# Performance work log

Measured on AMD Instinct MI355X. Metric: run time of the kernel, lower is better.

## Reference

```python
import jax, jax.numpy as jnp
import numpy as np

N_QUBITS = 10
QLCU_LAYERS = 2
GATE_LAYERS = 2
FEATURE_DIM = 256
OUTPUT_DIM = 1
BATCH = 2048
TWO_PI = float(2.0 * np.pi)
N_MEAS = 3 * N_QUBITS


def _ang(theta, B):
    # broadcast scalar or (B,) angle to (B,) float32
    return jnp.broadcast_to(jnp.asarray(theta, jnp.float32), (B,))


def _apply_1q(psi, U, wire):
    # psi: (B,)+(2,)*n ; U: (B,2,2) complex64
    pm = jnp.moveaxis(psi, wire + 1, -1)
    out = jnp.einsum('bij,b...j->b...i', U, pm)
    return jnp.moveaxis(out, -1, wire + 1)


def rx(psi, theta, wire):
    B = psi.shape[0]
    t = _ang(theta, B) * 0.5
    c = jnp.cos(t).astype(jnp.complex64)
    s = (-1j) * jnp.sin(t).astype(jnp.complex64)
    U = jnp.stack([jnp.stack([c, s], -1), jnp.stack([s, c], -1)], -2)
    return _apply_1q(psi, U, wire)


def ry(psi, theta, wire):
    B = psi.shape[0]
    t = _ang(theta, B) * 0.5
    c = jnp.cos(t).astype(jnp.complex64)
    s = jnp.sin(t).astype(jnp.complex64)
    U = jnp.stack([jnp.stack([c, -s], -1), jnp.stack([s, c], -1)], -2)
    return _apply_1q(psi, U, wire)


def rz(psi, theta, wire):
    # diagonal: e^{-i t/2}, e^{+i t/2}
    B = psi.shape[0]
    n = psi.ndim - 1
    t = _ang(theta, B) * 0.5
    ph = jnp.exp(1j * jnp.stack([-t, t], -1).astype(jnp.complex64))  # (B,2)
    pm = jnp.moveaxis(psi, wire + 1, -1)
    pm = pm * ph.reshape((B,) + (1,) * (n - 1) + (2,))
    return jnp.moveaxis(pm, -1, wire + 1)


def _mv2(psi, a, b):
    return jnp.moveaxis(psi, (a + 1, b + 1), (-2, -1))


def _mv2_back(pm, a, b):
    return jnp.moveaxis(pm, (-2, -1), (a + 1, b + 1))


def crz(psi, theta, control, target):
    # diagonal on (control,target): [1, 1, e^{-it/2}, e^{+it/2}]
    B = psi.shape[0]
    n = psi.ndim - 1
    t = (_ang(theta, B) * 0.5).astype(jnp.complex64)
    e_m = jnp.exp(-1j * t)
    e_p = jnp.exp(1j * t)
    one = jnp.ones_like(e_m)
    P = jnp.stack([jnp.stack([one, one], -1), jnp.stack([e_m, e_p], -1)], -2)  # (B,2,2)
    pm = _mv2(psi, control, target)
    pm = pm * P.reshape((B,) + (1,) * (n - 2) + (2, 2))
    return _mv2_back(pm, control, target)


def ising_xx(psi, theta, a, b):
    # exp(-i t/2 XX): cos(t/2) I - i sin(t/2) X(x)X (bit-flip both)
    B = psi.shape[0]
    n = psi.ndim - 1
    t = _ang(theta, B) * 0.5
    c = jnp.cos(t).astype(jnp.complex64).reshape((B,) + (1,) * n)
    s = jnp.sin(t).astype(jnp.complex64).reshape((B,) + (1,) * n)
    pm = _mv2(psi, a, b)
    out = c * pm - 1j * s * pm[..., ::-1, ::-1]
    return _mv2_back(out, a, b)


def ising_yy(psi, theta, a, b):
    # exp(-i t/2 YY): (YY psi)[ta,tb] = (-1 if ta==tb else +1) * psi[flip]
    B = psi.shape[0]
    n = psi.ndim - 1
    t = _ang(theta, B) * 0.5
    c = jnp.cos(t).astype(jnp.complex64).reshape((B,) + (1,) * n)
    s = jnp.sin(t).astype(jnp.complex64).reshape((B,) + (1,) * n)
    sign = jnp.array([[-1.0, 1.0], [1.0, -1.0]], jnp.complex64)
    pm = _mv2(psi, a, b)
    out = c * pm - 1j * s * sign * pm[..., ::-1, ::-1]
    return _mv2_back(out, a, b)


def measure_xyz(psi):
    # expvals [X0..X_{n-1}, Y0.., Z0..] -> (B, 3n) float32
    n = psi.ndim - 1
    xs, ys, zs = [], [], []
    for w in range(n):
        pm = jnp.moveaxis(psi, w + 1, -1)
        p0, p1 = pm[..., 0], pm[..., 1]
        axes = tuple(range(1, n))
        a = jnp.sum(jnp.conj(p0) * p1, axis=axes)
        xs.append(2.0 * jnp.real(a))
        ys.append(2.0 * jnp.imag(a))
        zs.append(jnp.sum(jnp.abs(p0) ** 2 - jnp.abs(p1) ** 2, axis=axes))
    return jnp.stack(xs + ys + zs, axis=1).astype(jnp.float32)


def selective_ssm(psi, qlcu, bpar, cpar, dtpar, n, layers):
    idx = 0
    for _ in range(layers):
        for i in range(n):
            psi = ry(psi, qlcu[:, idx], i); idx += 1
        for i in range(n):
            psi = ising_xx(psi, qlcu[:, idx], i, (i + 1) % n); idx += 1
        for i in range(n):
            psi = ry(psi, bpar[i], i)
        for i in range(n):
            psi = ry(psi, qlcu[:, idx], i); idx += 1
        for i in range(n):
            psi = ising_yy(psi, qlcu[:, idx], i, (i + 1) % n); idx += 1
        for i in range(n):
            psi = rz(psi, cpar[i], i)
        for i in range(n):
            psi = rx(psi, dtpar[i], i)
    return psi


def gating(psi, gp, n, layers):
    idx = 0
    for _ in range(layers):
        for i in range(n):
            psi = rx(psi, gp[idx], i); idx += 1
        for i in range(n - 1):
            psi = crz(psi, gp[idx], i, i + 1); idx += 1
        for i in range(n):
            psi = ry(psi, gp[idx], i); idx += 1
        if n > 1:
            psi = crz(psi, gp[idx], n - 1, 0); idx += 1
    return psi


def skip_circuit(psi, sp, n):
    idx = 0
    for i in range(n):
        psi = rx(psi, sp[idx], i); idx += 1
    for i in range(n):
        psi = ry(psi, sp[idx], i); idx += 1
    for i in range(n):
        psi = rz(psi, sp[idx], i); idx += 1
    return psi


def _forward(x, W_proj, b_proj, qlcu_base, gate_base, skip_base, b_params, c_params, dt_params,
             W1, b1, W2, b2, W3, b3, w1, w2, w3, W_out, b_out):
    B = x.shape[0]
    n = N_QUBITS
    proj = x @ W_proj.T + b_proj
    qlcu = jax.nn.sigmoid(proj) * TWO_PI + qlcu_base[None, :]
    psi0 = jnp.zeros((B, 2 ** n), jnp.complex64).at[:, 0].set(1.0).reshape((B,) + (2,) * n)
    m1 = measure_xyz(selective_ssm(psi0, qlcu, b_params, c_params, dt_params, n, QLCU_LAYERS))
    # branches 2/3 have batch-independent params and initial state -> compute once, broadcast
    psi1 = jnp.zeros((1, 2 ** n), jnp.complex64).at[:, 0].set(1.0).reshape((1,) + (2,) * n)
    m2 = jnp.broadcast_to(measure_xyz(gating(psi1, gate_base, n, GATE_LAYERS)), (B, N_MEAS))
    m3 = jnp.broadcast_to(measure_xyz(skip_circuit(psi1, skip_base, n)), (B, N_MEAS))
    y1 = m1 @ W1.T + b1
    y2 = m2 @ W2.T + b2
    y3 = m3 @ W3.T + b3
    comb = w1 * y1 + w2 * y2 + w3 * y3
    return comb @ W_out.T + b_out


def setup_inputs() -> dict:
    key = jax.random.key(0)
    ks = jax.random.split(key, 17)
    nq = N_QUBITS
    n_qlcu = 4 * nq * QLCU_LAYERS
    n_gate = 4 * nq * GATE_LAYERS
    n_skip = 3 * nq
    lim_p = 1.0 / np.sqrt(FEATURE_DIM)
    lim_m = 1.0 / np.sqrt(N_MEAS)
    return dict(
        x=jax.random.normal(ks[0], (BATCH, FEATURE_DIM), jnp.float32),
        W_proj=jax.random.uniform(ks[1], (n_qlcu, FEATURE_DIM), jnp.float32, -lim_p, lim_p),
        b_proj=jax.random.uniform(ks[2], (n_qlcu,), jnp.float32, -lim_p, lim_p),
        qlcu_base=jax.random.uniform(ks[3], (n_qlcu,), jnp.float32, 0.0, TWO_PI),
        gate_base=jax.random.uniform(ks[4], (n_gate,), jnp.float32, 0.0, TWO_PI),
        skip_base=jax.random.uniform(ks[5], (n_skip,), jnp.float32, 0.0, TWO_PI),
        b_params=jax.random.uniform(ks[6], (nq,), jnp.float32, 0.0, TWO_PI),
        c_params=jax.random.uniform(ks[7], (nq,), jnp.float32, 0.0, TWO_PI),
        dt_params=jax.random.uniform(ks[8], (nq,), jnp.float32, 0.0, TWO_PI),
        W1=jax.random.uniform(ks[9], (N_MEAS, N_MEAS), jnp.float32, -lim_m, lim_m),
        b1=jax.random.uniform(ks[10], (N_MEAS,), jnp.float32, -lim_m, lim_m),
        W2=jax.random.uniform(ks[11], (N_MEAS, N_MEAS), jnp.float32, -lim_m, lim_m),
        b2=jax.random.uniform(ks[12], (N_MEAS,), jnp.float32, -lim_m, lim_m),
        W3=jax.random.uniform(ks[13], (N_MEAS, N_MEAS), jnp.float32, -lim_m, lim_m),
        b3=jax.random.uniform(ks[14], (N_MEAS,), jnp.float32, -lim_m, lim_m),
        w1=jnp.ones((1,), jnp.float32),
        w2=jnp.ones((1,), jnp.float32),
        w3=jnp.ones((1,), jnp.float32),
        W_out=jax.random.uniform(ks[15], (OUTPUT_DIM, N_MEAS), jnp.float32, -lim_m, lim_m),
        b_out=jax.random.uniform(ks[16], (OUTPUT_DIM,), jnp.float32, -lim_m, lim_m),
    )


def reference(x, W_proj, b_proj, qlcu_base, gate_base, skip_base, b_params, c_params, dt_params,
              W1, b1, W2, b2, W3, b3, w1, w2, w3, W_out, b_out):
    return _forward(x, W_proj, b_proj, qlcu_base, gate_base, skip_base, b_params, c_params, dt_params,
                    W1, b1, W2, b2, W3, b3, w1, w2, w3, W_out, b_out)
```

## Files before the change

kernel.cpp:

```cpp
#include <hip/hip_runtime.h>
#include <math.h>

#define TPB 320
#define TWO_PI_F 6.283185307179586f


#define ALLQ(OP) OP(0) OP(1) OP(2) OP(3) OP(4) OP(5) OP(6) OP(7) OP(8) OP(9)
#define ALLQ9(OP) OP(0) OP(1) OP(2) OP(3) OP(4) OP(5) OP(6) OP(7) OP(8)

template<int CTRL>
__device__ __forceinline__ float dppmv(float v) {
    return __builtin_bit_cast(float,
        __builtin_amdgcn_update_dpp(0, __builtin_bit_cast(int, v), CTRL, 0xF, 0xF, true));
}

template<int LM>
__device__ __forceinline__ float lx(float v, int lane) {
    (void)lane;
    if constexpr (LM == 1)       return dppmv<0xB1>(v);
    else if constexpr (LM == 2)  return dppmv<0x4E>(v);
    else if constexpr (LM == 3)  return dppmv<0x1B>(v);
    else if constexpr (LM == 4)  return dppmv<0x1B>(dppmv<0x141>(v));
    else if constexpr (LM == 6)  return dppmv<0xB1>(dppmv<0x141>(v));
    else if constexpr (LM == 8)  return dppmv<0x128>(v);
    else if constexpr (LM == 12) return dppmv<0x1B>(dppmv<0x140>(v));
    else                         return __shfl_xor(v, LM);
}


template<int W>
__device__ __forceinline__ void g_ry(float (&re)[16], float (&im)[16], float c, float s, int lane) {
    if constexpr (W <= 5) {
        constexpr int LM = 1 << (5 - W);
        const float ss = ((lane >> (5 - W)) & 1) ? s : -s;
        float pr[16], pi[16];
#pragma unroll
        for (int r = 0; r < 16; ++r) { pr[r] = lx<LM>(re[r], lane); pi[r] = lx<LM>(im[r], lane); }
#pragma unroll
        for (int r = 0; r < 16; ++r) {
            re[r] = fmaf(ss, pr[r], c * re[r]);
            im[r] = fmaf(ss, pi[r], c * im[r]);
        }
    } else {
        constexpr int MK = 1 << (9 - W);
#pragma unroll
        for (int r = 0; r < 16; ++r) {
            if ((r & MK) == 0) {
                const int r1 = r | MK;
                float r0 = re[r], i0 = im[r], r1v = re[r1], i1 = im[r1];
                re[r]  = fmaf(-s, r1v, c * r0);
                im[r]  = fmaf(-s, i1,  c * i0);
                re[r1] = fmaf( s, r0,  c * r1v);
                im[r1] = fmaf( s, i0,  c * i1);
            }
        }
    }
}

template<int W>
__device__ __forceinline__ void g_rx(float (&re)[16], float (&im)[16], float c, float s, int lane) {
    if constexpr (W <= 5) {
        constexpr int LM = 1 << (5 - W);
        float pr[16], pi[16];
#pragma unroll
        for (int r = 0; r < 16; ++r) { pr[r] = lx<LM>(re[r], lane); pi[r] = lx<LM>(im[r], lane); }
#pragma unroll
        for (int r = 0; r < 16; ++r) {
            re[r] = fmaf( s, pi[r], c * re[r]);
            im[r] = fmaf(-s, pr[r], c * im[r]);
        }
    } else {
        constexpr int MK = 1 << (9 - W);
#pragma unroll
        for (int r = 0; r < 16; ++r) {
            if ((r & MK) == 0) {
                const int r1 = r | MK;
                float r0 = re[r], i0 = im[r], r1v = re[r1], i1 = im[r1];
                re[r]  = fmaf( s, i1,  c * r0);
                im[r]  = fmaf(-s, r1v, c * i0);
                re[r1] = fmaf( s, i0,  c * r1v);
                im[r1] = fmaf(-s, r0,  c * i1);
            }
        }
    }
}

template<int W>
__device__ __forceinline__ void g_rz(float (&re)[16], float (&im)[16], float c, float s, int lane) {
    if constexpr (W <= 5) {
        const float sp = ((lane >> (5 - W)) & 1) ? s : -s;
#pragma unroll
        for (int r = 0; r < 16; ++r) {
            float rr = re[r], ii = im[r];
            re[r] = rr * c - ii * sp;
            im[r] = ii * c + rr * sp;
        }
    } else {
        constexpr int MK = 1 << (9 - W);
#pragma unroll
        for (int r = 0; r < 16; ++r) {
            const float sp = (r & MK) ? s : -s;
            float rr = re[r], ii = im[r];
            re[r] = rr * c - ii * sp;
            im[r] = ii * c + rr * sp;
        }
    }
}

template<int C, int T>
__device__ __forceinline__ void g_crz(float (&re)[16], float (&im)[16], float c, float s, int lane) {
#pragma unroll
    for (int r = 0; r < 16; ++r) {
        const int cb = (C <= 5) ? ((lane >> (5 - C)) & 1) : ((r >> (9 - C)) & 1);
        const int tb = (T <= 5) ? ((lane >> (5 - T)) & 1) : ((r >> (9 - T)) & 1);
        const float cc  = cb ? c : 1.f;
        const float sp2 = cb ? (tb ? s : -s) : 0.f;
        float rr = re[r], ii = im[r];
        re[r] = cc * rr - sp2 * ii;
        im[r] = cc * ii + sp2 * rr;
    }
}

template<int A, int Bq, bool YY>
__device__ __forceinline__ void g_xy(float (&re)[16], float (&im)[16], float c, float s, int lane) {
    constexpr int bpA = 9 - A, bpB = 9 - Bq;
    constexpr int LM   = ((bpA >= 4) ? (1 << (bpA - 4)) : 0) | ((bpB >= 4) ? (1 << (bpB - 4)) : 0);
    constexpr int LOCM = ((bpA < 4) ? (1 << bpA) : 0) | ((bpB < 4) ? (1 << bpB) : 0);
    float pr[16], pi[16];
#pragma unroll
    for (int r = 0; r < 16; ++r) {
        float vr = re[r ^ LOCM], vi = im[r ^ LOCM];
        if constexpr (LM != 0) { pr[r] = lx<LM>(vr, lane); pi[r] = lx<LM>(vi, lane); }
        else                   { pr[r] = vr; pi[r] = vi; }
    }
#pragma unroll
    for (int r = 0; r < 16; ++r) {
        float sg;
        if constexpr (YY) {
            const int bA = (A  <= 5) ? ((lane >> (5 - A )) & 1) : ((r >> (9 - A )) & 1);
            const int bB = (Bq <= 5) ? ((lane >> (5 - Bq)) & 1) : ((r >> (9 - Bq)) & 1);
            sg = (bA == bB) ? -s : s;
        } else sg = s;
        float rr = re[r], ii = im[r];
        re[r] = fmaf( sg, pi[r], c * rr);
        im[r] = fmaf(-sg, pr[r], c * ii);
    }
}

template<int W>
__device__ __forceinline__ void g_u1(float (&re)[16], float (&im)[16], const float* U, int lane) {
    const float u00r=U[0], u00i=U[1], u01r=U[2], u01i=U[3];
    const float u10r=U[4], u10i=U[5], u11r=U[6], u11i=U[7];
    if constexpr (W <= 5) {
        constexpr int LM = 1 << (5 - W);
        const int side = (lane >> (5 - W)) & 1;
        const float aR = side ? u11r : u00r, aI = side ? u11i : u00i;
        const float bR = side ? u10r : u01r, bI = side ? u10i : u01i;
        float pr[16], pi[16];
#pragma unroll
        for (int r = 0; r < 16; ++r) { pr[r] = lx<LM>(re[r], lane); pi[r] = lx<LM>(im[r], lane); }
#pragma unroll
        for (int r = 0; r < 16; ++r) {
            float rr = re[r], ii = im[r];
            float nr = aR * rr; nr = fmaf(-aI, ii, nr); nr = fmaf(bR, pr[r], nr); nr = fmaf(-bI, pi[r], nr);
            float ni = aR * ii; ni = fmaf( aI, rr, ni); ni = fmaf(bR, pi[r], ni); ni = fmaf( bI, pr[r], ni);
            re[r] = nr; im[r] = ni;
        }
    } else {
        constexpr int MK = 1 << (9 - W);
#pragma unroll
        for (int r = 0; r < 16; ++r) {
            if ((r & MK) == 0) {
                const int r1 = r | MK;
                float r0 = re[r], i0 = im[r], r1v = re[r1], i1 = im[r1];
                float a = u00r*r0; a = fmaf(-u00i, i0, a); a = fmaf(u01r, r1v, a); a = fmaf(-u01i, i1, a);
                float b = u00r*i0; b = fmaf( u00i, r0, b); b = fmaf(u01r, i1,  b); b = fmaf( u01i, r1v, b);
                float c = u10r*r0; c = fmaf(-u10i, i0, c); c = fmaf(u11r, r1v, c); c = fmaf(-u11i, i1, c);
                float d = u10r*i0; d = fmaf( u10i, r0, d); d = fmaf(u11r, i1,  d); d = fmaf( u11i, r1v, d);
                re[r] = a; im[r] = b; re[r1] = c; im[r1] = d;
            }
        }
    }
}


__device__ __forceinline__ void g_ry2_01(float (&re)[16], float (&im)[16],
                                         float c0, float s0, float c1, float s1, int lane) {
    float ar[16], ai[16], br[16], bi[16], cr2[16], ci2[16];
#pragma unroll
    for (int r = 0; r < 16; ++r) { ar[r] = lx<32>(re[r], lane); ai[r] = lx<32>(im[r], lane); }
#pragma unroll
    for (int r = 0; r < 16; ++r) { br[r] = lx<16>(re[r], lane); bi[r] = lx<16>(im[r], lane); }
#pragma unroll
    for (int r = 0; r < 16; ++r) { cr2[r] = lx<48>(re[r], lane); ci2[r] = lx<48>(im[r], lane); }
    const float sg0 = ((lane >> 5) & 1) ? s0 : -s0;
    const float sg1 = ((lane >> 4) & 1) ? s1 : -s1;
    const float k0 = c0 * c1, k1 = c1 * sg0, k2 = c0 * sg1, k3 = sg0 * sg1;
#pragma unroll
    for (int r = 0; r < 16; ++r) {
        float o_r = k0 * re[r];
        o_r = fmaf(k1, ar[r], o_r); o_r = fmaf(k2, br[r], o_r); o_r = fmaf(k3, cr2[r], o_r);
        float o_i = k0 * im[r];
        o_i = fmaf(k1, ai[r], o_i); o_i = fmaf(k2, bi[r], o_i); o_i = fmaf(k3, ci2[r], o_i);
        re[r] = o_r; im[r] = o_i;
    }
}

__device__ __forceinline__ void g_u2_01(float (&re)[16], float (&im)[16],
                                        const float* U0, const float* U1, int lane) {
    const int b0 = (lane >> 5) & 1, b1 = (lane >> 4) & 1;
    const float u0o_r = U0[(b0*2+b0)*2],       u0o_i = U0[(b0*2+b0)*2+1];
    const float u0f_r = U0[(b0*2+(b0^1))*2],   u0f_i = U0[(b0*2+(b0^1))*2+1];
    const float u1o_r = U1[(b1*2+b1)*2],       u1o_i = U1[(b1*2+b1)*2+1];
    const float u1f_r = U1[(b1*2+(b1^1))*2],   u1f_i = U1[(b1*2+(b1^1))*2+1];
    const float K00r = u0o_r*u1o_r - u0o_i*u1o_i, K00i = u0o_r*u1o_i + u0o_i*u1o_r;
    const float K01r = u0o_r*u1f_r - u0o_i*u1f_i, K01i = u0o_r*u1f_i + u0o_i*u1f_r;
    const float K10r = u0f_r*u1o_r - u0f_i*u1o_i, K10i = u0f_r*u1o_i + u0f_i*u1o_r;
    const float K11r = u0f_r*u1f_r - u0f_i*u1f_i, K11i = u0f_r*u1f_i + u0f_i*u1f_r;
    float ar[16], ai[16], br[16], bi[16], cr2[16], ci2[16];
#pragma unroll
    for (int r = 0; r < 16; ++r) { ar[r] = lx<32>(re[r], lane); ai[r] = lx<32>(im[r], lane); }
#pragma unroll
    for (int r = 0; r < 16; ++r) { br[r] = lx<16>(re[r], lane); bi[r] = lx<16>(im[r], lane); }
#pragma unroll
    for (int r = 0; r < 16; ++r) { cr2[r] = lx<48>(re[r], lane); ci2[r] = lx<48>(im[r], lane); }
#pragma unroll
    for (int r = 0; r < 16; ++r) {
        float rr = re[r], ii = im[r];
        float o_r = K00r * rr;         o_r = fmaf(-K00i, ii, o_r);
        o_r = fmaf(K01r, br[r], o_r);  o_r = fmaf(-K01i, bi[r], o_r);
        o_r = fmaf(K10r, ar[r], o_r);  o_r = fmaf(-K10i, ai[r], o_r);
        o_r = fmaf(K11r, cr2[r], o_r); o_r = fmaf(-K11i, ci2[r], o_r);
        float o_i = K00r * ii;         o_i = fmaf(K00i, rr, o_i);
        o_i = fmaf(K01r, bi[r], o_i);  o_i = fmaf(K01i, br[r], o_i);
        o_i = fmaf(K10r, ai[r], o_i);  o_i = fmaf(K10i, ar[r], o_i);
        o_i = fmaf(K11r, ci2[r], o_i); o_i = fmaf(K11i, cr2[r], o_i);
        re[r] = o_r; im[r] = o_i;
    }
}

__device__ __forceinline__ void g_ring2(float (&re)[16], float (&im)[16],
                                        float ca, float sa, float cb, float sb,
                                        bool yy, int lane) {
    float ar[16], ai[16], br[16], bi[16], cr2[16], ci2[16];
#pragma unroll
    for (int r = 0; r < 16; ++r) { ar[r] = lx<24>(re[r], lane); ai[r] = lx<24>(im[r], lane); }
#pragma unroll
    for (int r = 0; r < 16; ++r) { br[r] = lx<32>(re[r ^ 1], lane); bi[r] = lx<32>(im[r ^ 1], lane); }
#pragma unroll
    for (int r = 0; r < 16; ++r) { cr2[r] = lx<56>(re[r ^ 1], lane); ci2[r] = lx<56>(im[r ^ 1], lane); }
    float ka, kb0, kb1, kab0, kab1;
    if (yy) {
        const bool ea = (((lane >> 4) & 1) == ((lane >> 3) & 1));
        const float sga = ea ? -sa : sa;
        const int b0l = (lane >> 5) & 1;
        const float sgb0 = (0 == b0l) ? -sb : sb;
        const float sgb1 = (1 == b0l) ? -sb : sb;
        ka = cb * sga; kb0 = ca * sgb0; kb1 = ca * sgb1;
        kab0 = sga * sgb0; kab1 = sga * sgb1;
    } else {
        ka = cb * sa; kb0 = kb1 = ca * sb; kab0 = kab1 = sa * sb;
    }
    const float k0 = ca * cb;
#pragma unroll
    for (int r = 0; r < 16; ++r) {
        const float kb  = (r & 1) ? kb1  : kb0;
        const float kab = (r & 1) ? kab1 : kab0;
        float rr = re[r], ii = im[r];
        float o_r = k0 * rr;
        o_r = fmaf(ka, ai[r], o_r); o_r = fmaf(kb, bi[r], o_r); o_r = fmaf(-kab, cr2[r], o_r);
        float o_i = k0 * ii;
        o_i = fmaf(-ka, ar[r], o_i); o_i = fmaf(-kb, br[r], o_i); o_i = fmaf(-kab, ci2[r], o_i);
        re[r] = o_r; im[r] = o_i;
    }
}

__device__ __forceinline__ float wred(float v, int lane) {
    v += lx<1>(v, lane); v += lx<2>(v, lane); v += lx<4>(v, lane);
    v += lx<8>(v, lane); v += lx<16>(v, lane); v += lx<32>(v, lane);
    return v;
}

template<int W>
__device__ __forceinline__ void meas_q(const float (&re)[16], const float (&im)[16], int lane,
                                       float& X, float& Y, float& Z) {
    float xa = 0.f, ya = 0.f, za = 0.f;
    if constexpr (W <= 5) {
        constexpr int LM = 1 << (5 - W);
        const float sg = ((lane >> (5 - W)) & 1) ? -1.f : 1.f;
        float pr[16], pi[16];
#pragma unroll
        for (int r = 0; r < 16; ++r) { pr[r] = lx<LM>(re[r], lane); pi[r] = lx<LM>(im[r], lane); }
#pragma unroll
        for (int r = 0; r < 16; ++r) {
            xa = fmaf(re[r], pr[r], xa); xa = fmaf(im[r], pi[r], xa);
            ya = fmaf(re[r], pi[r], ya); ya = fmaf(-im[r], pr[r], ya);
            za = fmaf(re[r], re[r], za); za = fmaf(im[r], im[r], za);
        }
        ya *= sg; za *= sg;
    } else {
        constexpr int MK = 1 << (9 - W);
#pragma unroll
        for (int r = 0; r < 16; ++r) {
            if ((r & MK) == 0) {
                const int r1 = r | MK;
                xa += 2.f * (re[r] * re[r1] + im[r] * im[r1]);
                ya += 2.f * (re[r] * im[r1] - im[r] * re[r1]);
                za += (re[r] * re[r] + im[r] * im[r]) - (re[r1] * re[r1] + im[r1] * im[r1]);
            }
        }
    }
    X = wred(xa, lane); Y = wred(ya, lane); Z = wred(za, lane);
}

__device__ __forceinline__ void init_state(float (&re)[16], float (&im)[16], int lane) {
#pragma unroll
    for (int r = 0; r < 16; ++r) { re[r] = 0.f; im[r] = 0.f; }
    if (lane == 0) re[0] = 1.f;
}


__device__ void branch_gating(const float* __restrict__ gb,
                              const float* __restrict__ b1,
                              const float* __restrict__ W2, const float* __restrict__ b2,
                              const float* __restrict__ w1p, const float* __restrict__ w2p,
                              const float* __restrict__ Wout, const float* __restrict__ bout,
                              float* __restrict__ ws_c, int lane) {
    float re[16], im[16];
    const bool act = lane < 30;
    const int kk = act ? lane : 0;
    float y2 = 0.f;

    init_state(re, im, lane);
    for (int L = 0; L < 2; ++L) {
        const int g0 = L * 30;
#define G_RX(i) { float s_, c_; __sincosf(0.5f * gb[g0 + i], &s_, &c_); g_rx<i>(re, im, c_, s_, lane); }
        ALLQ(G_RX)
#undef G_RX
#define G_CRZ(i) { float s_, c_; __sincosf(0.5f * gb[g0 + 10 + i], &s_, &c_); g_crz<i, i + 1>(re, im, c_, s_, lane); }
        ALLQ9(G_CRZ)
#undef G_CRZ
#define G_RY(i) { float s_, c_; __sincosf(0.5f * gb[g0 + 19 + i], &s_, &c_); g_ry<i>(re, im, c_, s_, lane); }
        ALLQ(G_RY)
#undef G_RY
        { float s_, c_; __sincosf(0.5f * gb[g0 + 29], &s_, &c_); g_crz<9, 0>(re, im, c_, s_, lane); }
    }
#define G_M2(w) { float X, Y, Z; meas_q<w>(re, im, lane, X, Y, Z); \
        y2 = fmaf(X, W2[kk * 30 + w], y2); y2 = fmaf(Y, W2[kk * 30 + 10 + w], y2); y2 = fmaf(Z, W2[kk * 30 + 20 + w], y2); }
    ALLQ(G_M2)
#undef G_M2

    const float w1v = w1p[0], w2v = w2p[0];
    float vk = act ? Wout[kk] * (w1v * b1[kk] + w2v * (b2[kk] + y2)) : 0.f;
    vk = wred(vk, lane);
    if (lane == 0) ws_c[0] = vk + bout[0];
}

__device__ void branch_skip(const float* __restrict__ sp,
                            const float* __restrict__ W3, const float* __restrict__ b3,
                            const float* __restrict__ w3p,
                            const float* __restrict__ Wout,
                            float* __restrict__ ws_c, int lane) {
    float re[16], im[16];
    const bool act = lane < 30;
    const int kk = act ? lane : 0;
    float y3 = 0.f;

    init_state(re, im, lane);
#define G_RXS(i) { float s_, c_; __sincosf(0.5f * sp[i], &s_, &c_); g_rx<i>(re, im, c_, s_, lane); }
    ALLQ(G_RXS)
#undef G_RXS
#define G_RYS(i) { float s_, c_; __sincosf(0.5f * sp[10 + i], &s_, &c_); g_ry<i>(re, im, c_, s_, lane); }
    ALLQ(G_RYS)
#undef G_RYS
#define G_RZS(i) { float s_, c_; __sincosf(0.5f * sp[20 + i], &s_, &c_); g_rz<i>(re, im, c_, s_, lane); }
    ALLQ(G_RZS)
#undef G_RZS
#define G_M3(w) { float X, Y, Z; meas_q<w>(re, im, lane, X, Y, Z); \
        y3 = fmaf(X, W3[kk * 30 + w], y3); y3 = fmaf(Y, W3[kk * 30 + 10 + w], y3); y3 = fmaf(Z, W3[kk * 30 + 20 + w], y3); }
    ALLQ(G_M3)
#undef G_M3

    const float w3v = w3p[0];
    float vk = act ? Wout[kk] * (w3v * (b3[kk] + y3)) : 0.f;
    vk = wred(vk, lane);
    if (lane == 0) ws_c[0] = vk;
}


__global__ void __launch_bounds__(TPB) k_main(
    const float* __restrict__ x, const float* __restrict__ Wp,
    const float* __restrict__ bp_, const float* __restrict__ qb,
    const float* __restrict__ bpar, const float* __restrict__ cpar, const float* __restrict__ dtpar,
    const float* __restrict__ gb, const float* __restrict__ sp,
    const float* __restrict__ W1, const float* __restrict__ b1,
    const float* __restrict__ W2, const float* __restrict__ b2,
    const float* __restrict__ W3, const float* __restrict__ b3,
    const float* __restrict__ w1p, const float* __restrict__ w2p, const float* __restrict__ w3p,
    const float* __restrict__ Wout, const float* __restrict__ bout,
    float* __restrict__ ws, int B) {

    const int wv = threadIdx.x >> 6, lane = threadIdx.x & 63;

    if (wv == 4) {
        if (blockIdx.x == 0) {
            branch_gating(gb, b1, W2, b2, w1p, w2p, Wout, bout, ws + B, lane);
            if (gridDim.x == 1) branch_skip(sp, W3, b3, w3p, Wout, ws + B + 1, lane);
        } else if (blockIdx.x == 1) {
            branch_skip(sp, W3, b3, w3p, Wout, ws + B + 1, lane);
        }
        return;
    }

    const int b = blockIdx.x * 4 + wv;
    const int bb = (b < B) ? b : (B - 1);

    __shared__ float proj[4][80];
    __shared__ float ac1[4][10], as1[4][10], ac2[4][10], as2[4][10];
    __shared__ float gc[4][60], gs[4][60];
    __shared__ float ub[4][80];
    __shared__ float uraw[4][32], uu[4][32];

    const int sub = lane & 15, grp = lane >> 4;
    float4 xv[4];
    {
        const float* xr = x + (size_t)bb * 256 + sub * 16;
#pragma unroll
        for (int j = 0; j < 4; ++j) xv[j] = reinterpret_cast<const float4*>(xr)[j];
    }
#pragma unroll 4
    for (int p = 0; p < 20; ++p) {
        const int row = p * 4 + grp;
        const float* wr = Wp + (size_t)row * 256 + sub * 16;
        float acc = 0.f;
#pragma unroll
        for (int j = 0; j < 4; ++j) {
            float4 w4 = reinterpret_cast<const float4*>(wr)[j];
            acc = fmaf(xv[j].x, w4.x, acc); acc = fmaf(xv[j].y, w4.y, acc);
            acc = fmaf(xv[j].z, w4.z, acc); acc = fmaf(xv[j].w, w4.w, acc);
        }
        acc += lx<1>(acc, lane); acc += lx<2>(acc, lane);
        acc += lx<4>(acc, lane); acc += lx<8>(acc, lane);
        if (sub == 0) proj[wv][row] = acc;
    }

    {
#define DO_ANGLE(IDX) { \
        const int idx = (IDX); \
        float ang = TWO_PI_F / (1.f + __expf(-(proj[wv][idx] + bp_[idx]))) + qb[idx]; \
        const int l = (idx >= 40) ? 1 : 0; \
        const int p = idx - 40 * l; \
        float s_, c_; \
        if (p < 10) { \
            __sincosf(0.5f * ang, &s_, &c_); \
            if (l == 0) { ac1[wv][p] = c_; as1[wv][p] = s_; } \
            else        { ac2[wv][p] = c_; as2[wv][p] = s_; } \
        } else if (p < 20) { \
            __sincosf(0.5f * ang, &s_, &c_); \
            gc[wv][l * 30 + p - 10] = c_; gs[wv][l * 30 + p - 10] = s_; \
        } else if (p < 30) { \
            __sincosf(0.5f * (ang + bpar[p - 20]), &s_, &c_); \
            gc[wv][l * 30 + 10 + p - 20] = c_; gs[wv][l * 30 + 10 + p - 20] = s_; \
        } else { \
            __sincosf(0.5f * ang, &s_, &c_); \
            gc[wv][l * 30 + 20 + p - 30] = c_; gs[wv][l * 30 + 20 + p - 30] = s_; \
        } }
        DO_ANGLE(lane)
        if (lane < 16) DO_ANGLE(64 + lane)
#undef DO_ANGLE

        if (lane < 30) {
            float ut = 0.f;
            for (int k = 0; k < 30; ++k) ut = fmaf(Wout[k], W1[k * 30 + lane], ut);
            uraw[wv][lane] = w1p[0] * ut;
        }
        if (lane < 10) {
            float ca = ac2[wv][lane], sa = as2[wv][lane];
            float cg2, sg2, cd2, sd2;
            __sincosf(0.5f * cpar[lane],  &sg2, &cg2);
            __sincosf(0.5f * dtpar[lane], &sd2, &cd2);
            float A = ca * cd2, Bv = sa * sd2;
            float C = -sa * cd2, D = -ca * sd2;
            float E = sa * cd2,  F = -ca * sd2;
            float G = ca * cd2,  H = -sa * sd2;
            float* U = &ub[wv][lane * 8];
            U[0] = cg2 * A + sg2 * Bv;  U[1] = cg2 * Bv - sg2 * A;
            U[2] = cg2 * C - sg2 * D;   U[3] = sg2 * C + cg2 * D;
            U[4] = cg2 * E + sg2 * F;   U[5] = cg2 * F - sg2 * E;
            U[6] = cg2 * G - sg2 * H;   U[7] = sg2 * G + cg2 * H;

            float cg, sgf, cd, sdf;
            __sincosf(cpar[lane],  &sgf, &cg);
            __sincosf(dtpar[lane], &sdf, &cd);
            float uX = uraw[wv][lane], uY = uraw[wv][10 + lane], uZ = uraw[wv][20 + lane];
            uu[wv][lane]      =  uX * cg + uY * cd * sgf + uZ * sdf * sgf;
            uu[wv][10 + lane] = -uX * sgf + uY * cd * cg + uZ * sdf * cg;
            uu[wv][20 + lane] = -uY * sdf + uZ * cd;
        }
    }

    float re[16], im[16];
    {
        const float* AC = ac1[wv]; const float* AS = as1[wv];
        float pl = ((lane >> 5) & 1) ? AS[0] : AC[0];
        pl *= ((lane >> 4) & 1) ? AS[1] : AC[1];
        pl *= ((lane >> 3) & 1) ? AS[2] : AC[2];
        pl *= ((lane >> 2) & 1) ? AS[3] : AC[3];
        pl *= ((lane >> 1) & 1) ? AS[4] : AC[4];
        pl *= ( lane       & 1) ? AS[5] : AC[5];
#pragma unroll
        for (int r = 0; r < 16; ++r) {
            float p = ((r >> 3) & 1) ? AS[6] : AC[6];
            p *= ((r >> 2) & 1) ? AS[7] : AC[7];
            p *= ((r >> 1) & 1) ? AS[8] : AC[8];
            p *= ( r       & 1) ? AS[9] : AC[9];
            re[r] = pl * p; im[r] = 0.f;
        }
    }

    const float* GC = gc[wv]; const float* GS = gs[wv];

#define RING(base, YYf) \
    g_ring2(re, im, GC[(base)+1], GS[(base)+1], GC[(base)+9], GS[(base)+9], YYf, lane); \
    g_xy<2, 3, YYf>(re, im, GC[(base)+2], GS[(base)+2], lane); \
    g_xy<3, 4, YYf>(re, im, GC[(base)+3], GS[(base)+3], lane); \
    g_xy<4, 5, YYf>(re, im, GC[(base)+4], GS[(base)+4], lane); \
    g_xy<5, 6, YYf>(re, im, GC[(base)+5], GS[(base)+5], lane); \
    g_xy<6, 7, YYf>(re, im, GC[(base)+6], GS[(base)+6], lane); \
    g_xy<7, 8, YYf>(re, im, GC[(base)+7], GS[(base)+7], lane); \
    g_xy<8, 9, YYf>(re, im, GC[(base)+8], GS[(base)+8], lane); \
    g_xy<0, 1, YYf>(re, im, GC[(base)+0], GS[(base)+0], lane);

    RING(0, false)
    g_ry2_01(re, im, GC[10], GS[10], GC[11], GS[11], lane);
#define G_CD1(i) g_ry<i>(re, im, GC[10 + i], GS[10 + i], lane);
    G_CD1(2) G_CD1(3) G_CD1(4) G_CD1(5) G_CD1(6) G_CD1(7) G_CD1(8) G_CD1(9)
#undef G_CD1
    RING(20, true)
    g_u2_01(re, im, &ub[wv][0], &ub[wv][8], lane);
#define G_UB(i) g_u1<i>(re, im, &ub[wv][i * 8], lane);
    G_UB(2) G_UB(3) G_UB(4) G_UB(5) G_UB(6) G_UB(7) G_UB(8) G_UB(9)
#undef G_UB
    RING(30, false)
    g_ry2_01(re, im, GC[40], GS[40], GC[41], GS[41], lane);
#define G_CD2(i) g_ry<i>(re, im, GC[40 + i], GS[40 + i], lane);
    G_CD2(2) G_CD2(3) G_CD2(4) G_CD2(5) G_CD2(6) G_CD2(7) G_CD2(8) G_CD2(9)
#undef G_CD2
    RING(50, true)
#undef RING

    const float* U = uu[wv];
    float oacc = 0.f;

    float q0r[16], q0i[16], q1r[16], q1i[16];
#pragma unroll
    for (int r = 0; r < 16; ++r) { q0r[r] = lx<32>(re[r], lane); q0i[r] = lx<32>(im[r], lane); }
#pragma unroll
    for (int r = 0; r < 16; ++r) { q1r[r] = lx<16>(re[r], lane); q1i[r] = lx<16>(im[r], lane); }

    float n2[16], n2s = 0.f;
#pragma unroll
    for (int r = 0; r < 16; ++r) { n2[r] = fmaf(re[r], re[r], im[r] * im[r]); n2s += n2[r]; }

#define M_LANE(w, LM_) { \
        float pr[16], pi[16]; \
        _Pragma("unroll") \
        for (int r = 0; r < 16; ++r) { pr[r] = lx<LM_>(re[r], lane); pi[r] = lx<LM_>(im[r], lane); } \
        float xa = 0.f, ya = 0.f; \
        _Pragma("unroll") \
        for (int r = 0; r < 16; ++r) { \
            xa = fmaf(re[r], pr[r], xa); xa = fmaf(im[r], pi[r], xa); \
            ya = fmaf(re[r], pi[r], ya); ya = fmaf(-im[r], pr[r], ya); \
        } \
        const float sg = ((lane >> (5 - w)) & 1) ? -1.f : 1.f; \
        oacc = fmaf(xa, U[w], oacc); \
        oacc = fmaf(sg * ya, U[10 + w], oacc); \
        oacc = fmaf(sg * n2s, U[20 + w], oacc); }
    M_LANE(2, 8) M_LANE(3, 4) M_LANE(4, 2) M_LANE(5, 1)
#undef M_LANE

#define M_REG(w, MK) { \
        float xa = 0.f, ya = 0.f, za = 0.f; \
        _Pragma("unroll") \
        for (int r = 0; r < 16; ++r) { \
            if ((r & MK) == 0) { \
                const int r1 = r | MK; \
                xa = fmaf(re[r], re[r1], xa); xa = fmaf(im[r], im[r1], xa); \
                ya = fmaf(re[r], im[r1], ya); ya = fmaf(-im[r], re[r1], ya); \
                za += n2[r] - n2[r1]; \
            } } \
        oacc = fmaf(2.f * xa, U[w], oacc); \
        oacc = fmaf(2.f * ya, U[10 + w], oacc); \
        oacc = fmaf(za, U[20 + w], oacc); }
    M_REG(6, 8) M_REG(7, 4) M_REG(8, 2) M_REG(9, 1)
#undef M_REG

    {
        float xa = 0.f, ya = 0.f;
#pragma unroll
        for (int r = 0; r < 16; ++r) {
            xa = fmaf(re[r], q0r[r], xa); xa = fmaf(im[r], q0i[r], xa);
            ya = fmaf(re[r], q0i[r], ya); ya = fmaf(-im[r], q0r[r], ya);
        }
        const float sg = ((lane >> 5) & 1) ? -1.f : 1.f;
        oacc = fmaf(xa, U[0], oacc);
        oacc = fmaf(sg * ya, U[10], oacc);
        oacc = fmaf(sg * n2s, U[20], oacc);
    }
    {
        float xa = 0.f, ya = 0.f;
#pragma unroll
        for (int r = 0; r < 16; ++r) {
            xa = fmaf(re[r], q1r[r], xa); xa = fmaf(im[r], q1i[r], xa);
            ya = fmaf(re[r], q1i[r], ya); ya = fmaf(-im[r], q1r[r], ya);
        }
        const float sg = ((lane >> 4) & 1) ? -1.f : 1.f;
        oacc = fmaf(xa, U[1], oacc);
        oacc = fmaf(sg * ya, U[11], oacc);
        oacc = fmaf(sg * n2s, U[21], oacc);
    }

    oacc = wred(oacc, lane);
    if (lane == 0 && b < B) ws[b] = oacc;
}

__global__ void k_out(const float* __restrict__ ws, float* __restrict__ out, int B) {
    int i = blockIdx.x * blockDim.x + threadIdx.x;
    if (i < B) out[i] = ws[i] + ws[B] + ws[B + 1];
}

extern "C" void kernel_launch(void* const* d_in, const int* in_sizes, int n_in,
                              void* d_out, int out_size, void* d_ws, size_t ws_size,
                              hipStream_t stream) {
    const float* x         = (const float*)d_in[0];
    const float* W_proj    = (const float*)d_in[1];
    const float* b_proj    = (const float*)d_in[2];
    const float* qlcu_base = (const float*)d_in[3];
    const float* gate_base = (const float*)d_in[4];
    const float* skip_base = (const float*)d_in[5];
    const float* b_params  = (const float*)d_in[6];
    const float* c_params  = (const float*)d_in[7];
    const float* dt_params = (const float*)d_in[8];
    const float* W1    = (const float*)d_in[9];
    const float* b1    = (const float*)d_in[10];
    const float* W2    = (const float*)d_in[11];
    const float* b2    = (const float*)d_in[12];
    const float* W3    = (const float*)d_in[13];
    const float* b3    = (const float*)d_in[14];
    const float* w1    = (const float*)d_in[15];
    const float* w2    = (const float*)d_in[16];
    const float* w3    = (const float*)d_in[17];
    const float* W_out = (const float*)d_in[18];
    const float* b_out = (const float*)d_in[19];
    float* out = (float*)d_out;
    float* ws  = (float*)d_ws;

    const int B = in_sizes[0] / 256;
    const int nb = (B + 3) / 4;

    hipLaunchKernelGGL(k_main, dim3(nb), dim3(TPB), 0, stream,
                       x, W_proj, b_proj, qlcu_base, b_params, c_params, dt_params,
                       gate_base, skip_base, W1, b1, W2, b2, W3, b3, w1, w2, w3,
                       W_out, b_out, ws, B);
    hipLaunchKernelGGL(k_out, dim3((B + 255) / 256), dim3(256), 0, stream, ws, out, B);
}
```

Measured before the change: 55.87 us.

## Fold gating/skip branch readouts into weighted measurement and closed-form product state

The gating branch now folds Wout·W2 into a per-observable weight vector in shared memory and reuses the shared meas_fold routine, so it needs a single reduction instead of 30 separate wave reductions. Its first RX and RY pairs on qubits 0 and 1 are also merged into combined two-qubit gates. The skip branch, whose circuit is a product state of single-qubit rotations, is computed in closed form per qubit instead of simulating the full state vector. These branches run on a side wave, so the gain depends on whether that wave was on the critical path.

```diff
diff --git a/kernel.cpp b/kernel.cpp
--- a/kernel.cpp
+++ b/kernel.cpp
@@ -202,6 +202,27 @@
         o_r = fmaf(k1, ar[r], o_r); o_r = fmaf(k2, br[r], o_r); o_r = fmaf(k3, cr2[r], o_r);
         float o_i = k0 * im[r];
         o_i = fmaf(k1, ai[r], o_i); o_i = fmaf(k2, bi[r], o_i); o_i = fmaf(k3, ci2[r], o_i);
+        re[r] = o_r; im[r] = o_i;
+    }
+}
+
+__device__ __forceinline__ void g_rx2_01(float (&re)[16], float (&im)[16],
+                                         float c0, float s0, float c1, float s1, int lane) {
+    float ar[16], ai[16], br[16], bi[16], cr2[16], ci2[16];
+#pragma unroll
+    for (int r = 0; r < 16; ++r) { ar[r] = lx<32>(re[r], lane); ai[r] = lx<32>(im[r], lane); }
+#pragma unroll
+    for (int r = 0; r < 16; ++r) { br[r] = lx<16>(re[r], lane); bi[r] = lx<16>(im[r], lane); }
+#pragma unroll
+    for (int r = 0; r < 16; ++r) { cr2[r] = lx<48>(re[r], lane); ci2[r] = lx<48>(im[r], lane); }
+    const float k0 = c0 * c1, kA = c1 * s0, kB = c0 * s1, kC = s0 * s1;
+#pragma unroll
+    for (int r = 0; r < 16; ++r) {
+        float rr = re[r], ii = im[r];
+        float o_r = k0 * rr;
+        o_r = fmaf(kA, ai[r], o_r); o_r = fmaf(kB, bi[r], o_r); o_r = fmaf(-kC, cr2[r], o_r);
+        float o_i = k0 * ii;
+        o_i = fmaf(-kA, ar[r], o_i); o_i = fmaf(-kB, br[r], o_i); o_i = fmaf(-kC, ci2[r], o_i);
         re[r] = o_r; im[r] = o_i;
     }
 }
@@ -281,36 +302,77 @@
     return v;
 }
 
-template<int W>
-__device__ __forceinline__ void meas_q(const float (&re)[16], const float (&im)[16], int lane,
-                                       float& X, float& Y, float& Z) {
-    float xa = 0.f, ya = 0.f, za = 0.f;
-    if constexpr (W <= 5) {
-        constexpr int LM = 1 << (5 - W);
-        const float sg = ((lane >> (5 - W)) & 1) ? -1.f : 1.f;
-        float pr[16], pi[16];
-#pragma unroll
-        for (int r = 0; r < 16; ++r) { pr[r] = lx<LM>(re[r], lane); pi[r] = lx<LM>(im[r], lane); }
-#pragma unroll
-        for (int r = 0; r < 16; ++r) {
-            xa = fmaf(re[r], pr[r], xa); xa = fmaf(im[r], pi[r], xa);
-            ya = fmaf(re[r], pi[r], ya); ya = fmaf(-im[r], pr[r], ya);
-            za = fmaf(re[r], re[r], za); za = fmaf(im[r], im[r], za);
-        }
-        ya *= sg; za *= sg;
-    } else {
-        constexpr int MK = 1 << (9 - W);
-#pragma unroll
-        for (int r = 0; r < 16; ++r) {
-            if ((r & MK) == 0) {
-                const int r1 = r | MK;
-                xa += 2.f * (re[r] * re[r1] + im[r] * im[r1]);
-                ya += 2.f * (re[r] * im[r1] - im[r] * re[r1]);
-                za += (re[r] * re[r] + im[r] * im[r]) - (re[r1] * re[r1] + im[r1] * im[r1]);
-            }
-        }
-    }
-    X = wred(xa, lane); Y = wred(ya, lane); Z = wred(za, lane);
+__device__ float meas_fold(const float (&re)[16], const float (&im)[16],
+                           const float* __restrict__ V, int lane) {
+    float oacc = 0.f;
+    float q0r[16], q0i[16], q1r[16], q1i[16];
+#pragma unroll
+    for (int r = 0; r < 16; ++r) { q0r[r] = lx<32>(re[r], lane); q0i[r] = lx<32>(im[r], lane); }
+#pragma unroll
+    for (int r = 0; r < 16; ++r) { q1r[r] = lx<16>(re[r], lane); q1i[r] = lx<16>(im[r], lane); }
+
+    float n2[16], n2s = 0.f;
+#pragma unroll
+    for (int r = 0; r < 16; ++r) { n2[r] = fmaf(re[r], re[r], im[r] * im[r]); n2s += n2[r]; }
+
+#define M_LANE(w, LM_) { \
+        float pr[16], pi[16]; \
+        _Pragma("unroll") \
+        for (int r = 0; r < 16; ++r) { pr[r] = lx<LM_>(re[r], lane); pi[r] = lx<LM_>(im[r], lane); } \
+        float xa = 0.f, ya = 0.f; \
+        _Pragma("unroll") \
+        for (int r = 0; r < 16; ++r) { \
+            xa = fmaf(re[r], pr[r], xa); xa = fmaf(im[r], pi[r], xa); \
+            ya = fmaf(re[r], pi[r], ya); ya = fmaf(-im[r], pr[r], ya); \
+        } \
+        const float sg = ((lane >> (5 - w)) & 1) ? -1.f : 1.f; \
+        oacc = fmaf(xa, V[w], oacc); \
+        oacc = fmaf(sg * ya, V[10 + w], oacc); \
+        oacc = fmaf(sg * n2s, V[20 + w], oacc); }
+    M_LANE(2, 8) M_LANE(3, 4) M_LANE(4, 2) M_LANE(5, 1)
+#undef M_LANE
+
+#define M_REG(w, MK) { \
+        float xa = 0.f, ya = 0.f, za = 0.f; \
+        _Pragma("unroll") \
+        for (int r = 0; r < 16; ++r) { \
+            if ((r & MK) == 0) { \
+                const int r1 = r | MK; \
+                xa = fmaf(re[r], re[r1], xa); xa = fmaf(im[r], im[r1], xa); \
+                ya = fmaf(re[r], im[r1], ya); ya = fmaf(-im[r], re[r1], ya); \
+                za += n2[r] - n2[r1]; \
+            } } \
+        oacc = fmaf(2.f * xa, V[w], oacc); \
+        oacc = fmaf(2.f * ya, V[10 + w], oacc); \
+        oacc = fmaf(za, V[20 + w], oacc); }
+    M_REG(6, 8) M_REG(7, 4) M_REG(8, 2) M_REG(9, 1)
+#undef M_REG
+
+    {
+        float xa = 0.f, ya = 0.f;
+#pragma unroll
+        for (int r = 0; r < 16; ++r) {
+            xa = fmaf(re[r], q0r[r], xa); xa = fmaf(im[r], q0i[r], xa);
+            ya = fmaf(re[r], q0i[r], ya); ya = fmaf(-im[r], q0r[r], ya);
+        }
+        const float sg = ((lane >> 5) & 1) ? -1.f : 1.f;
+        oacc = fmaf(xa, V[0], oacc);
+        oacc = fmaf(sg * ya, V[10], oacc);
+        oacc = fmaf(sg * n2s, V[20], oacc);
+    }
+    {
+        float xa = 0.f, ya = 0.f;
+#pragma unroll
+        for (int r = 0; r < 16; ++r) {
+            xa = fmaf(re[r], q1r[r], xa); xa = fmaf(im[r], q1i[r], xa);
+            ya = fmaf(re[r], q1i[r], ya); ya = fmaf(-im[r], q1r[r], ya);
+        }
+        const float sg = ((lane >> 4) & 1) ? -1.f : 1.f;
+        oacc = fmaf(xa, V[1], oacc);
+        oacc = fmaf(sg * ya, V[11], oacc);
+        oacc = fmaf(sg * n2s, V[21], oacc);
+    }
+    return oacc;
 }
 
 __device__ __forceinline__ void init_state(float (&re)[16], float (&im)[16], int lane) {
@@ -318,71 +380,78 @@
     for (int r = 0; r < 16; ++r) { re[r] = 0.f; im[r] = 0.f; }
     if (lane == 0) re[0] = 1.f;
 }
-
 
 __device__ void branch_gating(const float* __restrict__ gb,
                               const float* __restrict__ b1,
                               const float* __restrict__ W2, const float* __restrict__ b2,
                               const float* __restrict__ w1p, const float* __restrict__ w2p,
                               const float* __restrict__ Wout, const float* __restrict__ bout,
-                              float* __restrict__ ws_c, int lane) {
+                              float* __restrict__ vbr, float* __restrict__ ws_c, int lane) {
+    const float w1v = w1p[0], w2v = w2p[0];
+    float bias = 0.f;
+    if (lane < 30) {
+        float v = 0.f;
+        for (int k = 0; k < 30; ++k) v = fmaf(Wout[k], W2[k * 30 + lane], v);
+        vbr[lane] = w2v * v;
+        bias = Wout[lane] * (w1v * b1[lane] + w2v * b2[lane]);
+    }
+
     float re[16], im[16];
-    const bool act = lane < 30;
-    const int kk = act ? lane : 0;
-    float y2 = 0.f;
-
     init_state(re, im, lane);
     for (int L = 0; L < 2; ++L) {
         const int g0 = L * 30;
-#define G_RX(i) { float s_, c_; __sincosf(0.5f * gb[g0 + i], &s_, &c_); g_rx<i>(re, im, c_, s_, lane); }
-        ALLQ(G_RX)
-#undef G_RX
-#define G_CRZ(i) { float s_, c_; __sincosf(0.5f * gb[g0 + 10 + i], &s_, &c_); g_crz<i, i + 1>(re, im, c_, s_, lane); }
-        ALLQ9(G_CRZ)
-#undef G_CRZ
-#define G_RY(i) { float s_, c_; __sincosf(0.5f * gb[g0 + 19 + i], &s_, &c_); g_ry<i>(re, im, c_, s_, lane); }
-        ALLQ(G_RY)
-#undef G_RY
+        {
+            float c0_, s0_, c1_, s1_;
+            __sincosf(0.5f * gb[g0 + 0], &s0_, &c0_);
+            __sincosf(0.5f * gb[g0 + 1], &s1_, &c1_);
+            g_rx2_01(re, im, c0_, s0_, c1_, s1_, lane);
+        }
+#define BRX(i) { float s_, c_; __sincosf(0.5f * gb[g0 + i], &s_, &c_); g_rx<i>(re, im, c_, s_, lane); }
+        BRX(2) BRX(3) BRX(4) BRX(5) BRX(6) BRX(7) BRX(8) BRX(9)
+#undef BRX
+#define BCRZ(i) { float s_, c_; __sincosf(0.5f * gb[g0 + 10 + i], &s_, &c_); g_crz<i, i + 1>(re, im, c_, s_, lane); }
+        ALLQ9(BCRZ)
+#undef BCRZ
+        {
+            float c0_, s0_, c1_, s1_;
+            __sincosf(0.5f * gb[g0 + 19 + 0], &s0_, &c0_);
+            __sincosf(0.5f * gb[g0 + 19 + 1], &s1_, &c1_);
+            g_ry2_01(re, im, c0_, s0_, c1_, s1_, lane);
+        }
+#define BRY(i) { float s_, c_; __sincosf(0.5f * gb[g0 + 19 + i], &s_, &c_); g_ry<i>(re, im, c_, s_, lane); }
+        BRY(2) BRY(3) BRY(4) BRY(5) BRY(6) BRY(7) BRY(8) BRY(9)
+#undef BRY
         { float s_, c_; __sincosf(0.5f * gb[g0 + 29], &s_, &c_); g_crz<9, 0>(re, im, c_, s_, lane); }
     }
-#define G_M2(w) { float X, Y, Z; meas_q<w>(re, im, lane, X, Y, Z); \
-        y2 = fmaf(X, W2[kk * 30 + w], y2); y2 = fmaf(Y, W2[kk * 30 + 10 + w], y2); y2 = fmaf(Z, W2[kk * 30 + 20 + w], y2); }
-    ALLQ(G_M2)
-#undef G_M2
-
-    const float w1v = w1p[0], w2v = w2p[0];
-    float vk = act ? Wout[kk] * (w1v * b1[kk] + w2v * (b2[kk] + y2)) : 0.f;
-    vk = wred(vk, lane);
-    if (lane == 0) ws_c[0] = vk + bout[0];
+
+    float oacc = meas_fold(re, im, vbr, lane) + bias;
+    oacc = wred(oacc, lane);
+    if (lane == 0) ws_c[0] = oacc + bout[0];
 }
 
 __device__ void branch_skip(const float* __restrict__ sp,
-                            const float* __restrict__ W3, const float* __restrict__ b3,
+                            const float* __restrict__ W3, const float* __restrict__ b3v,
                             const float* __restrict__ w3p,
                             const float* __restrict__ Wout,
                             float* __restrict__ ws_c, int lane) {
-    float re[16], im[16];
-    const bool act = lane < 30;
-    const int kk = act ? lane : 0;
-    float y3 = 0.f;
-
-    init_state(re, im, lane);
-#define G_RXS(i) { float s_, c_; __sincosf(0.5f * sp[i], &s_, &c_); g_rx<i>(re, im, c_, s_, lane); }
-    ALLQ(G_RXS)
-#undef G_RXS
-#define G_RYS(i) { float s_, c_; __sincosf(0.5f * sp[10 + i], &s_, &c_); g_ry<i>(re, im, c_, s_, lane); }
-    ALLQ(G_RYS)
-#undef G_RYS
-#define G_RZS(i) { float s_, c_; __sincosf(0.5f * sp[20 + i], &s_, &c_); g_rz<i>(re, im, c_, s_, lane); }
-    ALLQ(G_RZS)
-#undef G_RZS
-#define G_M3(w) { float X, Y, Z; meas_q<w>(re, im, lane, X, Y, Z); \
-        y3 = fmaf(X, W3[kk * 30 + w], y3); y3 = fmaf(Y, W3[kk * 30 + 10 + w], y3); y3 = fmaf(Z, W3[kk * 30 + 20 + w], y3); }
-    ALLQ(G_M3)
-#undef G_M3
-
-    const float w3v = w3p[0];
-    float vk = act ? Wout[kk] * (w3v * (b3[kk] + y3)) : 0.f;
+    float vk = 0.f;
+    if (lane < 30) {
+        const int q = (lane < 10) ? lane : ((lane < 20) ? lane - 10 : lane - 20);
+        float c1, s1, c2, s2, c3, s3;
+        __sincosf(0.5f * sp[q],      &s1, &c1);
+        __sincosf(0.5f * sp[10 + q], &s2, &c2);
+        __sincosf(0.5f * sp[20 + q], &s3, &c3);
+        float a2r = c2 * c1, a2i = s2 * s1, b2r = s2 * c1, b2i = -c2 * s1;
+        float a3r = fmaf(a2i,  s3, a2r * c3), a3i = fmaf(-a2r, s3, a2i * c3);
+        float b3r = fmaf(-b2i, s3, b2r * c3), b3i = fmaf( b2r, s3, b2i * c3);
+        float m;
+        if (lane < 10)      m = 2.f * (a3r * b3r + a3i * b3i);
+        else if (lane < 20) m = 2.f * (a3r * b3i - a3i * b3r);
+        else                m = (a3r * a3r + a3i * a3i) - (b3r * b3r + b3i * b3i);
+        float v = 0.f;
+        for (int k = 0; k < 30; ++k) v = fmaf(Wout[k], W3[k * 30 + lane], v);
+        vk = w3p[0] * fmaf(m, v, Wout[lane] * b3v[lane]);
+    }
     vk = wred(vk, lane);
     if (lane == 0) ws_c[0] = vk;
 }
@@ -402,9 +471,11 @@
 
     const int wv = threadIdx.x >> 6, lane = threadIdx.x & 63;
 
+    __shared__ float vbr[32];
+
     if (wv == 4) {
         if (blockIdx.x == 0) {
-            branch_gating(gb, b1, W2, b2, w1p, w2p, Wout, bout, ws + B, lane);
+            branch_gating(gb, b1, W2, b2, w1p, w2p, Wout, bout, vbr, ws + B, lane);
             if (gridDim.x == 1) branch_skip(sp, W3, b3, w3p, Wout, ws + B + 1, lane);
         } else if (blockIdx.x == 1) {
             branch_skip(sp, W3, b3, w3p, Wout, ws + B + 1, lane);
@@ -549,77 +620,7 @@
     RING(50, true)
 #undef RING
 
-    const float* U = uu[wv];
-    float oacc = 0.f;
-
-    float q0r[16], q0i[16], q1r[16], q1i[16];
-#pragma unroll
-    for (int r = 0; r < 16; ++r) { q0r[r] = lx<32>(re[r], lane); q0i[r] = lx<32>(im[r], lane); }
-#pragma unroll
-    for (int r = 0; r < 16; ++r) { q1r[r] = lx<16>(re[r], lane); q1i[r] = lx<16>(im[r], lane); }
-
-    float n2[16], n2s = 0.f;
-#pragma unroll
-    for (int r = 0; r < 16; ++r) { n2[r] = fmaf(re[r], re[r], im[r] * im[r]); n2s += n2[r]; }
-
-#define M_LANE(w, LM_) { \
-        float pr[16], pi[16]; \
-        _Pragma("unroll") \
-        for (int r = 0; r < 16; ++r) { pr[r] = lx<LM_>(re[r], lane); pi[r] = lx<LM_>(im[r], lane); } \
-        float xa = 0.f, ya = 0.f; \
-        _Pragma("unroll") \
-        for (int r = 0; r < 16; ++r) { \
-            xa = fmaf(re[r], pr[r], xa); xa = fmaf(im[r], pi[r], xa); \
-            ya = fmaf(re[r], pi[r], ya); ya = fmaf(-im[r], pr[r], ya); \
-        } \
-        const float sg = ((lane >> (5 - w)) & 1) ? -1.f : 1.f; \
-        oacc = fmaf(xa, U[w], oacc); \
-        oacc = fmaf(sg * ya, U[10 + w], oacc); \
-        oacc = fmaf(sg * n2s, U[20 + w], oacc); }
-    M_LANE(2, 8) M_LANE(3, 4) M_LANE(4, 2) M_LANE(5, 1)
-#undef M_LANE
-
-#define M_REG(w, MK) { \
-        float xa = 0.f, ya = 0.f, za = 0.f; \
-        _Pragma("unroll") \
-        for (int r = 0; r < 16; ++r) { \
-            if ((r & MK) == 0) { \
-                const int r1 = r | MK; \
-                xa = fmaf(re[r], re[r1], xa); xa = fmaf(im[r], im[r1], xa); \
-                ya = fmaf(re[r], im[r1], ya); ya = fmaf(-im[r], re[r1], ya); \
-                za += n2[r] - n2[r1]; \
-            } } \
-        oacc = fmaf(2.f * xa, U[w], oacc); \
-        oacc = fmaf(2.f * ya, U[10 + w], oacc); \
-        oacc = fmaf(za, U[20 + w], oacc); }
-    M_REG(6, 8) M_REG(7, 4) M_REG(8, 2) M_REG(9, 1)
-#undef M_REG
-
-    {
-        float xa = 0.f, ya = 0.f;
-#pragma unroll
-        for (int r = 0; r < 16; ++r) {
-            xa = fmaf(re[r], q0r[r], xa); xa = fmaf(im[r], q0i[r], xa);
-            ya = fmaf(re[r], q0i[r], ya); ya = fmaf(-im[r], q0r[r], ya);
-        }
-        const float sg = ((lane >> 5) & 1) ? -1.f : 1.f;
-        oacc = fmaf(xa, U[0], oacc);
-        oacc = fmaf(sg * ya, U[10], oacc);
-        oacc = fmaf(sg * n2s, U[20], oacc);
-    }
-    {
-        float xa = 0.f, ya = 0.f;
-#pragma unroll
-        for (int r = 0; r < 16; ++r) {
-            xa = fmaf(re[r], q1r[r], xa); xa = fmaf(im[r], q1i[r], xa);
-            ya = fmaf(re[r], q1i[r], ya); ya = fmaf(-im[r], q1r[r], ya);
-        }
-        const float sg = ((lane >> 4) & 1) ? -1.f : 1.f;
-        oacc = fmaf(xa, U[1], oacc);
-        oacc = fmaf(sg * ya, U[11], oacc);
-        oacc = fmaf(sg * n2s, U[21], oacc);
-    }
-
+    float oacc = meas_fold(re, im, uu[wv], lane);
     oacc = wred(oacc, lane);
     if (lane == 0 && b < B) ws[b] = oacc;
 }
```

After: 48.59 us. 1.15x faster.
